# Kernel tuning notes

Hardware: AMD Instinct MI355X
Metric: run time of the kernel (lower is better)

The kernel has to match this reference:

```python
import jax, jax.numpy as jnp
import numpy as np

BATCH, DEPTH, N_MEM = 4096, 1024, 16384

def setup_inputs() -> dict:
    key = jax.random.key(0)
    kx, kw = jax.random.split(key)
    x = jax.random.normal(kx, (BATCH, DEPTH), dtype=jnp.float32)
    W = jax.random.normal(kw, (N_MEM, DEPTH), dtype=jnp.float32) * (1.0 / np.sqrt(DEPTH))
    return {"x": x, "W": W}

def reference(x, W):
    # scores: [batch, n] = x @ W^T
    scores = jnp.einsum('bd,nd->bn', x, W)
    # activation over the memory axis (modern Hopfield retrieval = softmax)
    attn = jax.nn.softmax(scores, axis=-1)
    # retrieve: [batch, depth] = attn @ W
    return jnp.einsum('bn,nd->bd', attn, W)
```

## Files before the change

kernel.cpp:

```cpp
#include <hip/hip_runtime.h>
#include <hip/hip_bf16.h>

typedef __attribute__((ext_vector_type(4))) float f32x4;
typedef __attribute__((ext_vector_type(8))) short bf16x8;
typedef __attribute__((ext_vector_type(8))) unsigned short u16x8;
typedef unsigned short u16;

#define B_ROWS 4096
#define DEPTH  1024
#define N_MEM  16384
#define QB     32
#define NB     256

#define XPERM_OFF   0ull
#define WPERM_OFF   8388608ull
#define WTPERM_OFF  41943040ull
#define OPART_OFF   75497472ull
#define ML_OFF      109051904ull
#define WS_NEED_SPLIT   109117440ull

__device__ __forceinline__ u16 f2bf(float f) {
    union { float f; unsigned int u; } x; x.f = f;
    unsigned int u = x.u;
    unsigned int r = (u + 0x7fffu + ((u >> 16) & 1u)) >> 16;
    return (u16)r;
}

__global__ __launch_bounds__(256) void perm_rows_kernel(const float* __restrict__ src,
                                                        u16* __restrict__ dst) {
    int g  = blockIdx.x * 256 + threadIdx.x;
    int l  = g & 63;
    int kk = (g >> 6) & 31;
    int ng = g >> 11;
    int lr = l & 15, lg = l >> 4;
    const float* p = src + (size_t)(ng * 16 + lr) * DEPTH + kk * 32 + lg * 8;
    f32x4 a = *(const f32x4*)p;
    f32x4 b = *(const f32x4*)(p + 4);
    u16x8 v;
    v[0] = f2bf(a[0]); v[1] = f2bf(a[1]); v[2] = f2bf(a[2]); v[3] = f2bf(a[3]);
    v[4] = f2bf(b[0]); v[5] = f2bf(b[1]); v[6] = f2bf(b[2]); v[7] = f2bf(b[3]);
    *(u16x8*)(dst + (size_t)g * 8) = v;
}

__global__ __launch_bounds__(256) void perm_wt_kernel(const float* __restrict__ src,
                                                      u16* __restrict__ dst) {
    int g   = blockIdx.x * 256 + threadIdx.x;
    int l   = g & 63;
    int kkn = (g >> 6) & 511;
    int dg  = g >> 15;
    int lr = l & 15, lg = l >> 4;
    int d  = dg * 16 + lr;
    int n0 = kkn * 32 + lg * 8;
    u16x8 v;
#pragma unroll
    for (int j = 0; j < 8; ++j)
        v[j] = f2bf(src[(size_t)(n0 + j) * DEPTH + d]);
    *(u16x8*)(dst + (size_t)g * 8) = v;
}

template <int NSPLIT>
__global__ __launch_bounds__(512, 2) void hop_main(const u16* __restrict__ xperm,
                                                   const u16* __restrict__ wperm,
                                                   const u16* __restrict__ wtperm,
                                                   float* __restrict__ opart,
                                                   float* __restrict__ mlbuf,
                                                   float* __restrict__ outd) {
    constexpr int NCHUNK = N_MEM / NSPLIT;
    constexpr int NTILES = NCHUNK / NB;

    __shared__ u16  xls[2 * 32 * 64 * 8];
    __shared__ u16  Pl[QB][NB + 8];
    __shared__ float maxbuf[QB][8];
    __shared__ float sumbuf[QB][8];

    const int tid = threadIdx.x;
    const int w = tid >> 6, l = tid & 63;
    const int lr = l & 15, lg = l >> 4;
    const int bid = blockIdx.x;
    const int c  = (NSPLIT == 1) ? 0 : (bid & (NSPLIT - 1));
    const int rb = (NSPLIT == 1) ? bid : (bid >> 1);

    {
        const u16x8* sp = ((const u16x8*)xperm) + (size_t)rb * 4096;
        u16x8* dp = (u16x8*)xls;
#pragma unroll
        for (int i = 0; i < 8; ++i) dp[tid + i * 512] = sp[tid + i * 512];
    }

    float mreg[2][4], lreg[2][4];
#pragma unroll
    for (int rg = 0; rg < 2; ++rg)
#pragma unroll
        for (int r = 0; r < 4; ++r) { mreg[rg][r] = -1e30f; lreg[rg][r] = 0.0f; }
    f32x4 oacc[2][8];
#pragma unroll
    for (int rg = 0; rg < 2; ++rg)
#pragma unroll
        for (int d8 = 0; d8 < 8; ++d8) oacc[rg][d8] = (f32x4){0.f, 0.f, 0.f, 0.f};

    __syncthreads();

    const bf16x8* xv = (const bf16x8*)xls;

    for (int t = 0; t < NTILES; ++t) {
        f32x4 s[2][2];
#pragma unroll
        for (int rg = 0; rg < 2; ++rg)
#pragma unroll
            for (int j = 0; j < 2; ++j) s[rg][j] = (f32x4){0.f, 0.f, 0.f, 0.f};
        const int ngb = c * (NCHUNK / 16) + t * (NB / 16) + 2 * w;
        const bf16x8* w0 = ((const bf16x8*)wperm) + ((size_t)ngb * 32) * 64 + l;
        const bf16x8* w1 = w0 + 32 * 64;
#pragma unroll
        for (int kk = 0; kk < 32; ++kk) {
            bf16x8 a0 = xv[kk * 64 + l];
            bf16x8 a1 = xv[(32 + kk) * 64 + l];
            bf16x8 b0 = w0[kk * 64];
            bf16x8 b1 = w1[kk * 64];
            s[0][0] = __builtin_amdgcn_mfma_f32_16x16x32_bf16(a0, b0, s[0][0], 0, 0, 0);
            s[0][1] = __builtin_amdgcn_mfma_f32_16x16x32_bf16(a0, b1, s[0][1], 0, 0, 0);
            s[1][0] = __builtin_amdgcn_mfma_f32_16x16x32_bf16(a1, b0, s[1][0], 0, 0, 0);
            s[1][1] = __builtin_amdgcn_mfma_f32_16x16x32_bf16(a1, b1, s[1][1], 0, 0, 0);
        }

        float tmax[2][4];
#pragma unroll
        for (int rg = 0; rg < 2; ++rg)
#pragma unroll
            for (int r = 0; r < 4; ++r) tmax[rg][r] = fmaxf(s[rg][0][r], s[rg][1][r]);
#pragma unroll
        for (int off = 1; off < 16; off <<= 1) {
#pragma unroll
            for (int rg = 0; rg < 2; ++rg)
#pragma unroll
                for (int r = 0; r < 4; ++r)
                    tmax[rg][r] = fmaxf(tmax[rg][r], __shfl_xor(tmax[rg][r], off));
        }
        if (lr == 0) {
#pragma unroll
            for (int rg = 0; rg < 2; ++rg)
#pragma unroll
                for (int r = 0; r < 4; ++r) maxbuf[rg * 16 + lg * 4 + r][w] = tmax[rg][r];
        }
        __syncthreads();

        float alpha[2][4], pv[2][2][4], tsum[2][4];
#pragma unroll
        for (int rg = 0; rg < 2; ++rg)
#pragma unroll
            for (int r = 0; r < 4; ++r) {
                const f32x4* mb = (const f32x4*)(&maxbuf[rg * 16 + lg * 4 + r][0]);
                f32x4 a4 = mb[0], b4 = mb[1];
                float tm = fmaxf(fmaxf(fmaxf(a4[0], a4[1]), fmaxf(a4[2], a4[3])),
                                 fmaxf(fmaxf(b4[0], b4[1]), fmaxf(b4[2], b4[3])));
                float mn = fmaxf(mreg[rg][r], tm);
                alpha[rg][r] = __expf(mreg[rg][r] - mn);
                mreg[rg][r]  = mn;
                pv[rg][0][r] = __expf(s[rg][0][r] - mn);
                pv[rg][1][r] = __expf(s[rg][1][r] - mn);
                tsum[rg][r] = pv[rg][0][r] + pv[rg][1][r];
                lreg[rg][r] *= alpha[rg][r];
            }
#pragma unroll
        for (int off = 1; off < 16; off <<= 1) {
#pragma unroll
            for (int rg = 0; rg < 2; ++rg)
#pragma unroll
                for (int r = 0; r < 4; ++r)
                    tsum[rg][r] += __shfl_xor(tsum[rg][r], off);
        }
        if (lr == 0) {
#pragma unroll
            for (int rg = 0; rg < 2; ++rg)
#pragma unroll
                for (int r = 0; r < 4; ++r) sumbuf[rg * 16 + lg * 4 + r][w] = tsum[rg][r];
        }
#pragma unroll
        for (int rg = 0; rg < 2; ++rg)
#pragma unroll
            for (int d8 = 0; d8 < 8; ++d8)
#pragma unroll
                for (int r = 0; r < 4; ++r) oacc[rg][d8][r] *= alpha[rg][r];
#pragma unroll
        for (int rg = 0; rg < 2; ++rg)
#pragma unroll
            for (int r = 0; r < 4; ++r) {
                int R = rg * 16 + lg * 4 + r;
                Pl[R][32 * w + lr]      = f2bf(pv[rg][0][r]);
                Pl[R][32 * w + 16 + lr] = f2bf(pv[rg][1][r]);
            }
        __syncthreads();

#pragma unroll
        for (int rg = 0; rg < 2; ++rg)
#pragma unroll
            for (int r = 0; r < 4; ++r) {
                const f32x4* sb = (const f32x4*)(&sumbuf[rg * 16 + lg * 4 + r][0]);
                f32x4 a4 = sb[0], b4 = sb[1];
                lreg[rg][r] += (a4[0] + a4[1] + a4[2] + a4[3]) + (b4[0] + b4[1] + b4[2] + b4[3]);
            }

        const int kkb = c * (NCHUNK / 32) + t * (NB / 32);
        const bf16x8* wt0 = ((const bf16x8*)wtperm) + ((size_t)(w * 8) * 512 + kkb) * 64 + l;
#pragma unroll
        for (int kk = 0; kk < 8; ++kk) {
            bf16x8 pa0 = *(const bf16x8*)(&Pl[lr][kk * 32 + lg * 8]);
            bf16x8 pa1 = *(const bf16x8*)(&Pl[16 + lr][kk * 32 + lg * 8]);
#pragma unroll
            for (int d8 = 0; d8 < 8; ++d8) {
                bf16x8 wb = wt0[((size_t)d8 * 512 + kk) * 64];
                oacc[0][d8] = __builtin_amdgcn_mfma_f32_16x16x32_bf16(pa0, wb, oacc[0][d8], 0, 0, 0);
                oacc[1][d8] = __builtin_amdgcn_mfma_f32_16x16x32_bf16(pa1, wb, oacc[1][d8], 0, 0, 0);
            }
        }
    }

    if (NSPLIT == 1) {
        float inv[2][4];
#pragma unroll
        for (int rg = 0; rg < 2; ++rg)
#pragma unroll
            for (int r = 0; r < 4; ++r) inv[rg][r] = 1.0f / lreg[rg][r];
        float* op = outd + (size_t)rb * QB * DEPTH;
#pragma unroll
        for (int rg = 0; rg < 2; ++rg)
#pragma unroll
            for (int d8 = 0; d8 < 8; ++d8) {
                int d = w * 128 + d8 * 16 + lr;
#pragma unroll
                for (int r = 0; r < 4; ++r)
                    op[(size_t)(rg * 16 + lg * 4 + r) * DEPTH + d] = oacc[rg][d8][r] * inv[rg][r];
            }
    } else {
        float* op = opart + ((size_t)c * B_ROWS + rb * QB) * DEPTH;
#pragma unroll
        for (int rg = 0; rg < 2; ++rg)
#pragma unroll
            for (int d8 = 0; d8 < 8; ++d8) {
                int d = w * 128 + d8 * 16 + lr;
#pragma unroll
                for (int r = 0; r < 4; ++r)
                    op[(size_t)(rg * 16 + lg * 4 + r) * DEPTH + d] = oacc[rg][d8][r];
            }
        if (w == 0 && lr == 0) {
#pragma unroll
            for (int rg = 0; rg < 2; ++rg)
#pragma unroll
                for (int r = 0; r < 4; ++r) {
                    int R = rg * 16 + lg * 4 + r;
                    size_t base = ((size_t)c * B_ROWS + rb * QB + R) * 2;
                    mlbuf[base]     = mreg[rg][r];
                    mlbuf[base + 1] = lreg[rg][r];
                }
        }
    }
}

__global__ __launch_bounds__(256) void combine_kernel(const float* __restrict__ opart,
                                                      const float* __restrict__ mlbuf,
                                                      float* __restrict__ outd) {
    int idx = blockIdx.x * 256 + threadIdx.x;
    int b = idx >> 8;
    f32x4 o0 = ((const f32x4*)opart)[idx];
    f32x4 o1 = ((const f32x4*)opart)[idx + (B_ROWS * DEPTH / 4)];
    float m0 = mlbuf[(size_t)b * 2],            l0 = mlbuf[(size_t)b * 2 + 1];
    float m1 = mlbuf[((size_t)B_ROWS + b) * 2], l1 = mlbuf[((size_t)B_ROWS + b) * 2 + 1];
    float M = fmaxf(m0, m1);
    float e0 = __expf(m0 - M), e1 = __expf(m1 - M);
    float inv = 1.0f / (e0 * l0 + e1 * l1);
    ((f32x4*)outd)[idx] = (o0 * e0 + o1 * e1) * inv;
}

extern "C" void kernel_launch(void* const* d_in, const int* in_sizes, int n_in,
                              void* d_out, int out_size, void* d_ws, size_t ws_size,
                              hipStream_t stream) {
    (void)in_sizes; (void)n_in; (void)out_size;
    const float* x = (const float*)d_in[0];
    const float* W = (const float*)d_in[1];
    float* out = (float*)d_out;
    char* ws = (char*)d_ws;

    u16* xperm  = (u16*)(ws + XPERM_OFF);
    u16* wperm  = (u16*)(ws + WPERM_OFF);
    u16* wtperm = (u16*)(ws + WTPERM_OFF);

    perm_rows_kernel<<<2048, 256, 0, stream>>>(x, xperm);
    perm_rows_kernel<<<8192, 256, 0, stream>>>(W, wperm);
    perm_wt_kernel<<<8192, 256, 0, stream>>>(W, wtperm);

    if (ws_size >= WS_NEED_SPLIT) {
        float* opart = (float*)(ws + OPART_OFF);
        float* mlb   = (float*)(ws + ML_OFF);
        hop_main<2><<<(B_ROWS / QB) * 2, 512, 0, stream>>>(xperm, wperm, wtperm, opart, mlb, out);
        combine_kernel<<<4096, 256, 0, stream>>>(opart, mlb, out);
    } else {
        hop_main<1><<<B_ROWS / QB, 512, 0, stream>>>(xperm, wperm, wtperm, nullptr, nullptr, out);
    }
}
```

Measured before the change: 677.9 us.

## Widen query tile to 64 rows, shrink memory tile, add 4-way N split

Doubles the query-row block per workgroup (QB 32→64) and halves the memory tile (NB 256→128), so each W tile load is reused across four 16-row MFMA groups instead of two. This is meant to halve global W traffic per output row. It also adds a 4-way split over the memory axis, with a block-index swizzle, to keep the grid size up, plus a generic combine kernel. In exchange it doubles the per-thread output accumulators (oacc 4x8 f32x4) and LDS use, which risks spills and lower occupancy under launch_bounds(512,2). It also moves more partial-output traffic through the combine step.

```diff
diff --git a/kernel.cpp b/kernel.cpp
--- a/kernel.cpp
+++ b/kernel.cpp
@@ -9,15 +9,17 @@
 #define B_ROWS 4096
 #define DEPTH  1024
 #define N_MEM  16384
-#define QB     32
-#define NB     256
+#define QB     64
+#define NB     128
 
 #define XPERM_OFF   0ull
 #define WPERM_OFF   8388608ull
 #define WTPERM_OFF  41943040ull
 #define OPART_OFF   75497472ull
-#define ML_OFF      109051904ull
-#define WS_NEED_SPLIT   109117440ull
+#define ML4_OFF     142606336ull
+#define ML2_OFF     109051904ull
+#define WS_NEED_SPLIT4  142737408ull
+#define WS_NEED_SPLIT2  109117440ull
 
 __device__ __forceinline__ u16 f2bf(float f) {
     union { float f; unsigned int u; } x; x.f = f;
@@ -68,7 +70,7 @@
     constexpr int NCHUNK = N_MEM / NSPLIT;
     constexpr int NTILES = NCHUNK / NB;
 
-    __shared__ u16  xls[2 * 32 * 64 * 8];
+    __shared__ u16  xls[4 * 32 * 64 * 8];
     __shared__ u16  Pl[QB][NB + 8];
     __shared__ float maxbuf[QB][8];
     __shared__ float sumbuf[QB][8];
@@ -77,24 +79,26 @@
     const int w = tid >> 6, l = tid & 63;
     const int lr = l & 15, lg = l >> 4;
     const int bid = blockIdx.x;
-    const int c  = (NSPLIT == 1) ? 0 : (bid & (NSPLIT - 1));
-    const int rb = (NSPLIT == 1) ? bid : (bid >> 1);
+    int c, rb;
+    if (NSPLIT == 4)      { c = (bid & 7) >> 1; rb = ((bid >> 3) << 1) | (bid & 1); }
+    else if (NSPLIT == 2) { c = bid & 1;        rb = bid >> 1; }
+    else                  { c = 0;              rb = bid; }
 
     {
-        const u16x8* sp = ((const u16x8*)xperm) + (size_t)rb * 4096;
+        const u16x8* sp = ((const u16x8*)xperm) + (size_t)rb * 8192;
         u16x8* dp = (u16x8*)xls;
 #pragma unroll
-        for (int i = 0; i < 8; ++i) dp[tid + i * 512] = sp[tid + i * 512];
-    }
-
-    float mreg[2][4], lreg[2][4];
-#pragma unroll
-    for (int rg = 0; rg < 2; ++rg)
+        for (int i = 0; i < 16; ++i) dp[tid + i * 512] = sp[tid + i * 512];
+    }
+
+    float mreg[4][4], lreg[4][4];
+#pragma unroll
+    for (int rg = 0; rg < 4; ++rg)
 #pragma unroll
         for (int r = 0; r < 4; ++r) { mreg[rg][r] = -1e30f; lreg[rg][r] = 0.0f; }
-    f32x4 oacc[2][8];
-#pragma unroll
-    for (int rg = 0; rg < 2; ++rg)
+    f32x4 oacc[4][8];
+#pragma unroll
+    for (int rg = 0; rg < 4; ++rg)
 #pragma unroll
         for (int d8 = 0; d8 < 8; ++d8) oacc[rg][d8] = (f32x4){0.f, 0.f, 0.f, 0.f};
 
@@ -103,50 +107,44 @@
     const bf16x8* xv = (const bf16x8*)xls;
 
     for (int t = 0; t < NTILES; ++t) {
-        f32x4 s[2][2];
-#pragma unroll
-        for (int rg = 0; rg < 2; ++rg)
-#pragma unroll
-            for (int j = 0; j < 2; ++j) s[rg][j] = (f32x4){0.f, 0.f, 0.f, 0.f};
-        const int ngb = c * (NCHUNK / 16) + t * (NB / 16) + 2 * w;
-        const bf16x8* w0 = ((const bf16x8*)wperm) + ((size_t)ngb * 32) * 64 + l;
-        const bf16x8* w1 = w0 + 32 * 64;
+        f32x4 s[4];
+#pragma unroll
+        for (int rg = 0; rg < 4; ++rg) s[rg] = (f32x4){0.f, 0.f, 0.f, 0.f};
+        const int ngb = c * (NCHUNK / 16) + t * (NB / 16) + w;
+        const bf16x8* wp = ((const bf16x8*)wperm) + ((size_t)ngb * 32) * 64 + l;
 #pragma unroll
         for (int kk = 0; kk < 32; ++kk) {
-            bf16x8 a0 = xv[kk * 64 + l];
-            bf16x8 a1 = xv[(32 + kk) * 64 + l];
-            bf16x8 b0 = w0[kk * 64];
-            bf16x8 b1 = w1[kk * 64];
-            s[0][0] = __builtin_amdgcn_mfma_f32_16x16x32_bf16(a0, b0, s[0][0], 0, 0, 0);
-            s[0][1] = __builtin_amdgcn_mfma_f32_16x16x32_bf16(a0, b1, s[0][1], 0, 0, 0);
-            s[1][0] = __builtin_amdgcn_mfma_f32_16x16x32_bf16(a1, b0, s[1][0], 0, 0, 0);
-            s[1][1] = __builtin_amdgcn_mfma_f32_16x16x32_bf16(a1, b1, s[1][1], 0, 0, 0);
-        }
-
-        float tmax[2][4];
-#pragma unroll
-        for (int rg = 0; rg < 2; ++rg)
-#pragma unroll
-            for (int r = 0; r < 4; ++r) tmax[rg][r] = fmaxf(s[rg][0][r], s[rg][1][r]);
+            bf16x8 b = wp[kk * 64];
+            s[0] = __builtin_amdgcn_mfma_f32_16x16x32_bf16(xv[(0 * 32 + kk) * 64 + l], b, s[0], 0, 0, 0);
+            s[1] = __builtin_amdgcn_mfma_f32_16x16x32_bf16(xv[(1 * 32 + kk) * 64 + l], b, s[1], 0, 0, 0);
+            s[2] = __builtin_amdgcn_mfma_f32_16x16x32_bf16(xv[(2 * 32 + kk) * 64 + l], b, s[2], 0, 0, 0);
+            s[3] = __builtin_amdgcn_mfma_f32_16x16x32_bf16(xv[(3 * 32 + kk) * 64 + l], b, s[3], 0, 0, 0);
+        }
+
+        float tmax[4][4];
+#pragma unroll
+        for (int rg = 0; rg < 4; ++rg)
+#pragma unroll
+            for (int r = 0; r < 4; ++r) tmax[rg][r] = s[rg][r];
 #pragma unroll
         for (int off = 1; off < 16; off <<= 1) {
 #pragma unroll
-            for (int rg = 0; rg < 2; ++rg)
+            for (int rg = 0; rg < 4; ++rg)
 #pragma unroll
                 for (int r = 0; r < 4; ++r)
                     tmax[rg][r] = fmaxf(tmax[rg][r], __shfl_xor(tmax[rg][r], off));
         }
         if (lr == 0) {
 #pragma unroll
-            for (int rg = 0; rg < 2; ++rg)
+            for (int rg = 0; rg < 4; ++rg)
 #pragma unroll
                 for (int r = 0; r < 4; ++r) maxbuf[rg * 16 + lg * 4 + r][w] = tmax[rg][r];
         }
         __syncthreads();
 
-        float alpha[2][4], pv[2][2][4], tsum[2][4];
-#pragma unroll
-        for (int rg = 0; rg < 2; ++rg)
+        float alpha[4][4], pval[4][4], tsum[4][4];
+#pragma unroll
+        for (int rg = 0; rg < 4; ++rg)
 #pragma unroll
             for (int r = 0; r < 4; ++r) {
                 const f32x4* mb = (const f32x4*)(&maxbuf[rg * 16 + lg * 4 + r][0]);
@@ -156,43 +154,39 @@
                 float mn = fmaxf(mreg[rg][r], tm);
                 alpha[rg][r] = __expf(mreg[rg][r] - mn);
                 mreg[rg][r]  = mn;
-                pv[rg][0][r] = __expf(s[rg][0][r] - mn);
-                pv[rg][1][r] = __expf(s[rg][1][r] - mn);
-                tsum[rg][r] = pv[rg][0][r] + pv[rg][1][r];
+                pval[rg][r]  = __expf(s[rg][r] - mn);
+                tsum[rg][r]  = pval[rg][r];
                 lreg[rg][r] *= alpha[rg][r];
             }
 #pragma unroll
         for (int off = 1; off < 16; off <<= 1) {
 #pragma unroll
-            for (int rg = 0; rg < 2; ++rg)
+            for (int rg = 0; rg < 4; ++rg)
 #pragma unroll
                 for (int r = 0; r < 4; ++r)
                     tsum[rg][r] += __shfl_xor(tsum[rg][r], off);
         }
         if (lr == 0) {
 #pragma unroll
-            for (int rg = 0; rg < 2; ++rg)
+            for (int rg = 0; rg < 4; ++rg)
 #pragma unroll
                 for (int r = 0; r < 4; ++r) sumbuf[rg * 16 + lg * 4 + r][w] = tsum[rg][r];
         }
 #pragma unroll
-        for (int rg = 0; rg < 2; ++rg)
+        for (int rg = 0; rg < 4; ++rg)
 #pragma unroll
             for (int d8 = 0; d8 < 8; ++d8)
 #pragma unroll
                 for (int r = 0; r < 4; ++r) oacc[rg][d8][r] *= alpha[rg][r];
 #pragma unroll
-        for (int rg = 0; rg < 2; ++rg)
-#pragma unroll
-            for (int r = 0; r < 4; ++r) {
-                int R = rg * 16 + lg * 4 + r;
-                Pl[R][32 * w + lr]      = f2bf(pv[rg][0][r]);
-                Pl[R][32 * w + 16 + lr] = f2bf(pv[rg][1][r]);
-            }
+        for (int rg = 0; rg < 4; ++rg)
+#pragma unroll
+            for (int r = 0; r < 4; ++r)
+                Pl[rg * 16 + lg * 4 + r][16 * w + lr] = f2bf(pval[rg][r]);
         __syncthreads();
 
 #pragma unroll
-        for (int rg = 0; rg < 2; ++rg)
+        for (int rg = 0; rg < 4; ++rg)
 #pragma unroll
             for (int r = 0; r < 4; ++r) {
                 const f32x4* sb = (const f32x4*)(&sumbuf[rg * 16 + lg * 4 + r][0]);
@@ -200,30 +194,34 @@
                 lreg[rg][r] += (a4[0] + a4[1] + a4[2] + a4[3]) + (b4[0] + b4[1] + b4[2] + b4[3]);
             }
 
-        const int kkb = c * (NCHUNK / 32) + t * (NB / 32);
-        const bf16x8* wt0 = ((const bf16x8*)wtperm) + ((size_t)(w * 8) * 512 + kkb) * 64 + l;
-#pragma unroll
-        for (int kk = 0; kk < 8; ++kk) {
-            bf16x8 pa0 = *(const bf16x8*)(&Pl[lr][kk * 32 + lg * 8]);
-            bf16x8 pa1 = *(const bf16x8*)(&Pl[16 + lr][kk * 32 + lg * 8]);
+        const int kkn0 = c * (NCHUNK / 32) + t * (NB / 32);
+        const bf16x8* wt0 = ((const bf16x8*)wtperm) + ((size_t)(w * 8) * 512 + kkn0) * 64 + l;
+#pragma unroll
+        for (int kkp = 0; kkp < 4; ++kkp) {
+            bf16x8 pa[4];
+#pragma unroll
+            for (int rg = 0; rg < 4; ++rg)
+                pa[rg] = *(const bf16x8*)(&Pl[rg * 16 + lr][kkp * 32 + lg * 8]);
 #pragma unroll
             for (int d8 = 0; d8 < 8; ++d8) {
-                bf16x8 wb = wt0[((size_t)d8 * 512 + kk) * 64];
-                oacc[0][d8] = __builtin_amdgcn_mfma_f32_16x16x32_bf16(pa0, wb, oacc[0][d8], 0, 0, 0);
-                oacc[1][d8] = __builtin_amdgcn_mfma_f32_16x16x32_bf16(pa1, wb, oacc[1][d8], 0, 0, 0);
+                bf16x8 wb = wt0[((size_t)d8 * 512 + kkp) * 64];
+                oacc[0][d8] = __builtin_amdgcn_mfma_f32_16x16x32_bf16(pa[0], wb, oacc[0][d8], 0, 0, 0);
+                oacc[1][d8] = __builtin_amdgcn_mfma_f32_16x16x32_bf16(pa[1], wb, oacc[1][d8], 0, 0, 0);
+                oacc[2][d8] = __builtin_amdgcn_mfma_f32_16x16x32_bf16(pa[2], wb, oacc[2][d8], 0, 0, 0);
+                oacc[3][d8] = __builtin_amdgcn_mfma_f32_16x16x32_bf16(pa[3], wb, oacc[3][d8], 0, 0, 0);
             }
         }
     }
 
     if (NSPLIT == 1) {
-        float inv[2][4];
-#pragma unroll
-        for (int rg = 0; rg < 2; ++rg)
+        float inv[4][4];
+#pragma unroll
+        for (int rg = 0; rg < 4; ++rg)
 #pragma unroll
             for (int r = 0; r < 4; ++r) inv[rg][r] = 1.0f / lreg[rg][r];
         float* op = outd + (size_t)rb * QB * DEPTH;
 #pragma unroll
-        for (int rg = 0; rg < 2; ++rg)
+        for (int rg = 0; rg < 4; ++rg)
 #pragma unroll
             for (int d8 = 0; d8 < 8; ++d8) {
                 int d = w * 128 + d8 * 16 + lr;
@@ -234,7 +232,7 @@
     } else {
         float* op = opart + ((size_t)c * B_ROWS + rb * QB) * DEPTH;
 #pragma unroll
-        for (int rg = 0; rg < 2; ++rg)
+        for (int rg = 0; rg < 4; ++rg)
 #pragma unroll
             for (int d8 = 0; d8 < 8; ++d8) {
                 int d = w * 128 + d8 * 16 + lr;
@@ -244,7 +242,7 @@
             }
         if (w == 0 && lr == 0) {
 #pragma unroll
-            for (int rg = 0; rg < 2; ++rg)
+            for (int rg = 0; rg < 4; ++rg)
 #pragma unroll
                 for (int r = 0; r < 4; ++r) {
                     int R = rg * 16 + lg * 4 + r;
@@ -256,19 +254,30 @@
     }
 }
 
+template <int NS>
 __global__ __launch_bounds__(256) void combine_kernel(const float* __restrict__ opart,
                                                       const float* __restrict__ mlbuf,
                                                       float* __restrict__ outd) {
     int idx = blockIdx.x * 256 + threadIdx.x;
     int b = idx >> 8;
-    f32x4 o0 = ((const f32x4*)opart)[idx];
-    f32x4 o1 = ((const f32x4*)opart)[idx + (B_ROWS * DEPTH / 4)];
-    float m0 = mlbuf[(size_t)b * 2],            l0 = mlbuf[(size_t)b * 2 + 1];
-    float m1 = mlbuf[((size_t)B_ROWS + b) * 2], l1 = mlbuf[((size_t)B_ROWS + b) * 2 + 1];
-    float M = fmaxf(m0, m1);
-    float e0 = __expf(m0 - M), e1 = __expf(m1 - M);
-    float inv = 1.0f / (e0 * l0 + e1 * l1);
-    ((f32x4*)outd)[idx] = (o0 * e0 + o1 * e1) * inv;
+    float m[NS], lv[NS];
+    float M = -1e30f;
+#pragma unroll
+    for (int cc = 0; cc < NS; ++cc) {
+        m[cc]  = mlbuf[((size_t)cc * B_ROWS + b) * 2];
+        lv[cc] = mlbuf[((size_t)cc * B_ROWS + b) * 2 + 1];
+        M = fmaxf(M, m[cc]);
+    }
+    float denom = 0.f;
+    f32x4 acc = (f32x4){0.f, 0.f, 0.f, 0.f};
+#pragma unroll
+    for (int cc = 0; cc < NS; ++cc) {
+        float e = __expf(m[cc] - M);
+        denom += e * lv[cc];
+        f32x4 o = ((const f32x4*)opart)[idx + (size_t)cc * (B_ROWS * DEPTH / 4)];
+        acc += o * e;
+    }
+    ((f32x4*)outd)[idx] = acc * (1.0f / denom);
 }
 
 extern "C" void kernel_launch(void* const* d_in, const int* in_sizes, int n_in,
@@ -288,11 +297,16 @@
     perm_rows_kernel<<<8192, 256, 0, stream>>>(W, wperm);
     perm_wt_kernel<<<8192, 256, 0, stream>>>(W, wtperm);
 
-    if (ws_size >= WS_NEED_SPLIT) {
+    if (ws_size >= WS_NEED_SPLIT4) {
         float* opart = (float*)(ws + OPART_OFF);
-        float* mlb   = (float*)(ws + ML_OFF);
+        float* mlb   = (float*)(ws + ML4_OFF);
+        hop_main<4><<<(B_ROWS / QB) * 4, 512, 0, stream>>>(xperm, wperm, wtperm, opart, mlb, out);
+        combine_kernel<4><<<4096, 256, 0, stream>>>(opart, mlb, out);
+    } else if (ws_size >= WS_NEED_SPLIT2) {
+        float* opart = (float*)(ws + OPART_OFF);
+        float* mlb   = (float*)(ws + ML2_OFF);
         hop_main<2><<<(B_ROWS / QB) * 2, 512, 0, stream>>>(xperm, wperm, wtperm, opart, mlb, out);
-        combine_kernel<<<4096, 256, 0, stream>>>(opart, mlb, out);
+        combine_kernel<2><<<4096, 256, 0, stream>>>(opart, mlb, out);
     } else {
         hop_main<1><<<B_ROWS / QB, 512, 0, stream>>>(xperm, wperm, wtperm, nullptr, nullptr, out);
     }
```

Result: slower. 932.9 us (+37.6%).

## Batch W loads ahead of MFMAs and regroup split-block mapping

Applied to the files above, without the earlier changes.

Both GEMM inner loops are restructured. Global W fragments are now loaded in batches of four (QK) or eight (PV) before the corresponding MFMAs issue, with the outer loops marked unroll 1, so load latency can overlap and register pressure stays bounded. The block-to-(row block, chunk) mapping for the two-way split is changed so that four consecutive row blocks share the same N chunk, which is meant to improve L2 reuse of W across concurrently running blocks. Not fully unrolling reduces scheduling freedom, and the renames are cosmetic.

```diff
diff --git a/kernel.cpp b/kernel.cpp
--- a/kernel.cpp
+++ b/kernel.cpp
@@ -16,8 +16,8 @@
 #define WPERM_OFF   8388608ull
 #define WTPERM_OFF  41943040ull
 #define OPART_OFF   75497472ull
-#define ML_OFF      109051904ull
-#define WS_NEED_SPLIT   109117440ull
+#define ML2_OFF     109051904ull
+#define WS_NEED_SPLIT2  109117440ull
 
 __device__ __forceinline__ u16 f2bf(float f) {
     union { float f; unsigned int u; } x; x.f = f;
@@ -77,8 +77,9 @@
     const int w = tid >> 6, l = tid & 63;
     const int lr = l & 15, lg = l >> 4;
     const int bid = blockIdx.x;
-    const int c  = (NSPLIT == 1) ? 0 : (bid & (NSPLIT - 1));
-    const int rb = (NSPLIT == 1) ? bid : (bid >> 1);
+    int c, rb;
+    if (NSPLIT == 2)      { c = (bid & 7) >> 2; rb = ((bid >> 3) << 2) | (bid & 3); }
+    else                  { c = 0;              rb = bid; }
 
     {
         const u16x8* sp = ((const u16x8*)xperm) + (size_t)rb * 4096;
@@ -111,16 +112,24 @@
         const int ngb = c * (NCHUNK / 16) + t * (NB / 16) + 2 * w;
         const bf16x8* w0 = ((const bf16x8*)wperm) + ((size_t)ngb * 32) * 64 + l;
         const bf16x8* w1 = w0 + 32 * 64;
-#pragma unroll
-        for (int kk = 0; kk < 32; ++kk) {
-            bf16x8 a0 = xv[kk * 64 + l];
-            bf16x8 a1 = xv[(32 + kk) * 64 + l];
-            bf16x8 b0 = w0[kk * 64];
-            bf16x8 b1 = w1[kk * 64];
-            s[0][0] = __builtin_amdgcn_mfma_f32_16x16x32_bf16(a0, b0, s[0][0], 0, 0, 0);
-            s[0][1] = __builtin_amdgcn_mfma_f32_16x16x32_bf16(a0, b1, s[0][1], 0, 0, 0);
-            s[1][0] = __builtin_amdgcn_mfma_f32_16x16x32_bf16(a1, b0, s[1][0], 0, 0, 0);
-            s[1][1] = __builtin_amdgcn_mfma_f32_16x16x32_bf16(a1, b1, s[1][1], 0, 0, 0);
+#pragma unroll 1
+        for (int kk4 = 0; kk4 < 8; ++kk4) {
+            bf16x8 b0v[4], b1v[4];
+#pragma unroll
+            for (int j = 0; j < 4; ++j) {
+                b0v[j] = w0[(kk4 * 4 + j) * 64];
+                b1v[j] = w1[(kk4 * 4 + j) * 64];
+            }
+#pragma unroll
+            for (int j = 0; j < 4; ++j) {
+                const int kk = kk4 * 4 + j;
+                bf16x8 a0 = xv[kk * 64 + l];
+                bf16x8 a1 = xv[(32 + kk) * 64 + l];
+                s[0][0] = __builtin_amdgcn_mfma_f32_16x16x32_bf16(a0, b0v[j], s[0][0], 0, 0, 0);
+                s[0][1] = __builtin_amdgcn_mfma_f32_16x16x32_bf16(a0, b1v[j], s[0][1], 0, 0, 0);
+                s[1][0] = __builtin_amdgcn_mfma_f32_16x16x32_bf16(a1, b0v[j], s[1][0], 0, 0, 0);
+                s[1][1] = __builtin_amdgcn_mfma_f32_16x16x32_bf16(a1, b1v[j], s[1][1], 0, 0, 0);
+            }
         }
 
         float tmax[2][4];
@@ -144,7 +153,7 @@
         }
         __syncthreads();
 
-        float alpha[2][4], pv[2][2][4], tsum[2][4];
+        float alpha[2][4], pval[2][2][4], tsum[2][4];
 #pragma unroll
         for (int rg = 0; rg < 2; ++rg)
 #pragma unroll
@@ -156,9 +165,9 @@
                 float mn = fmaxf(mreg[rg][r], tm);
                 alpha[rg][r] = __expf(mreg[rg][r] - mn);
                 mreg[rg][r]  = mn;
-                pv[rg][0][r] = __expf(s[rg][0][r] - mn);
-                pv[rg][1][r] = __expf(s[rg][1][r] - mn);
-                tsum[rg][r] = pv[rg][0][r] + pv[rg][1][r];
+                pval[rg][0][r] = __expf(s[rg][0][r] - mn);
+                pval[rg][1][r] = __expf(s[rg][1][r] - mn);
+                tsum[rg][r] = pval[rg][0][r] + pval[rg][1][r];
                 lreg[rg][r] *= alpha[rg][r];
             }
 #pragma unroll
@@ -186,8 +195,8 @@
 #pragma unroll
             for (int r = 0; r < 4; ++r) {
                 int R = rg * 16 + lg * 4 + r;
-                Pl[R][32 * w + lr]      = f2bf(pv[rg][0][r]);
-                Pl[R][32 * w + 16 + lr] = f2bf(pv[rg][1][r]);
+                Pl[R][32 * w + lr]      = f2bf(pval[rg][0][r]);
+                Pl[R][32 * w + 16 + lr] = f2bf(pval[rg][1][r]);
             }
         __syncthreads();
 
@@ -200,17 +209,19 @@
                 lreg[rg][r] += (a4[0] + a4[1] + a4[2] + a4[3]) + (b4[0] + b4[1] + b4[2] + b4[3]);
             }
 
-        const int kkb = c * (NCHUNK / 32) + t * (NB / 32);
-        const bf16x8* wt0 = ((const bf16x8*)wtperm) + ((size_t)(w * 8) * 512 + kkb) * 64 + l;
-#pragma unroll
+        const int kkn0 = c * (NCHUNK / 32) + t * (NB / 32);
+        const bf16x8* wt0 = ((const bf16x8*)wtperm) + ((size_t)(w * 8) * 512 + kkn0) * 64 + l;
+#pragma unroll 1
         for (int kk = 0; kk < 8; ++kk) {
+            bf16x8 wb[8];
+#pragma unroll
+            for (int d8 = 0; d8 < 8; ++d8) wb[d8] = wt0[((size_t)d8 * 512 + kk) * 64];
             bf16x8 pa0 = *(const bf16x8*)(&Pl[lr][kk * 32 + lg * 8]);
             bf16x8 pa1 = *(const bf16x8*)(&Pl[16 + lr][kk * 32 + lg * 8]);
 #pragma unroll
             for (int d8 = 0; d8 < 8; ++d8) {
-                bf16x8 wb = wt0[((size_t)d8 * 512 + kk) * 64];
-                oacc[0][d8] = __builtin_amdgcn_mfma_f32_16x16x32_bf16(pa0, wb, oacc[0][d8], 0, 0, 0);
-                oacc[1][d8] = __builtin_amdgcn_mfma_f32_16x16x32_bf16(pa1, wb, oacc[1][d8], 0, 0, 0);
+                oacc[0][d8] = __builtin_amdgcn_mfma_f32_16x16x32_bf16(pa0, wb[d8], oacc[0][d8], 0, 0, 0);
+                oacc[1][d8] = __builtin_amdgcn_mfma_f32_16x16x32_bf16(pa1, wb[d8], oacc[1][d8], 0, 0, 0);
             }
         }
     }
@@ -288,9 +299,9 @@
     perm_rows_kernel<<<8192, 256, 0, stream>>>(W, wperm);
     perm_wt_kernel<<<8192, 256, 0, stream>>>(W, wtperm);
 
-    if (ws_size >= WS_NEED_SPLIT) {
+    if (ws_size >= WS_NEED_SPLIT2) {
         float* opart = (float*)(ws + OPART_OFF);
-        float* mlb   = (float*)(ws + ML_OFF);
+        float* mlb   = (float*)(ws + ML2_OFF);
         hop_main<2><<<(B_ROWS / QB) * 2, 512, 0, stream>>>(xperm, wperm, wtperm, opart, mlb, out);
         combine_kernel<<<4096, 256, 0, stream>>>(opart, mlb, out);
     } else {
```

Result: slower. 777.6 us (+14.7%).
